# Kernel tuning notes

Hardware: AMD Instinct MI355X
Metric: run time of the kernel (lower is better)

The kernel has to match this reference:

```python
import jax, jax.numpy as jnp
import numpy as np

LEAKY_SLOPE = 0.2

def _xavier(key, shape, gain=1.414):
    a = gain * np.sqrt(6.0 / (shape[0] + shape[1]))
    return jax.random.uniform(key, shape, minval=-a, maxval=a, dtype=jnp.float32)

C_IN, HID = 64, 128
S_SCALES = [25, 12, 5]
T_SCALES = [64, 32, 16]

def setup_inputs() -> dict:
    key = jax.random.key(0)
    ks = jax.random.split(key, 32)
    B, T, J = 256, 64, 25
    d = {}
    d["src"] = jax.random.normal(ks[0], (B, C_IN, T, J), dtype=jnp.float32)
    d["W"] = _xavier(ks[1], (C_IN, HID))
    for i in range(3):
        d[f"as_src{i}"] = _xavier(ks[2 + i], (HID, 1))
        d[f"as_dst{i}"] = _xavier(ks[5 + i], (HID, 1))
        d[f"at_src{i}"] = _xavier(ks[8 + i], (HID, 1))
        d[f"at_dst{i}"] = _xavier(ks[11 + i], (HID, 1))
    # DiffPool assignment linears: in_features -> next_scale
    d["Wsp0"] = _xavier(ks[14], (C_IN, S_SCALES[1])); d["bsp0"] = jnp.zeros((S_SCALES[1],), jnp.float32)
    d["Wsp1"] = _xavier(ks[15], (C_IN, S_SCALES[2])); d["bsp1"] = jnp.zeros((S_SCALES[2],), jnp.float32)
    d["Wtp0"] = _xavier(ks[16], (C_IN, T_SCALES[1])); d["btp0"] = jnp.zeros((T_SCALES[1],), jnp.float32)
    d["Wtp1"] = _xavier(ks[17], (C_IN, T_SCALES[2])); d["btp1"] = jnp.zeros((T_SCALES[2],), jnp.float32)
    return d


def _gat_attn(emb, a_src, a_dst):
    # emb: [N, n, H]; additive GAT scores -> [N, n, n]
    s = emb @ a_src            # [N, n, 1]
    t = emb @ a_dst            # [N, n, 1]
    return jax.nn.leaky_relu(s + jnp.swapaxes(t, -1, -2), LEAKY_SLOPE)


def _diffpool(x, attn, Wp, bp):
    # assignment S = softmax(Linear(A @ X)) : [N, n, n_next]
    S = jax.nn.softmax((attn @ x) @ Wp + bp, axis=-1)
    x_next = jnp.einsum('bnk,bnc->bkc', S, x)
    return x_next, S


def _branch(x0, W, a_srcs, a_dsts, pool_params):
    n_scales = len(a_srcs)
    attns, pools = [], []
    x_cur = x0
    for i in range(n_scales):
        emb = x_cur @ W
        attns.append(_gat_attn(emb, a_srcs[i], a_dsts[i]))
        if i < n_scales - 1:
            Wp, bp = pool_params[i]
            x_cur, S = _diffpool(x_cur, attns[i], Wp, bp)
            pools.append(S)
    fusion = attns[0]
    for i in range(1, n_scales):
        S = pools[0]
        for j in range(1, i):
            S = S @ pools[j]
        fusion = fusion + S @ attns[i] @ jnp.swapaxes(S, -1, -2)
    # dropout is identity in eval mode
    return jax.nn.softmax(fusion, axis=-1)


def reference(src, W, as_src0, as_src1, as_src2, as_dst0, as_dst1, as_dst2,
              at_src0, at_src1, at_src2, at_dst0, at_dst1, at_dst2,
              Wsp0, bsp0, Wsp1, bsp1, Wtp0, btp0, Wtp1, btp1):
    B, C_in, T, J = src.shape
    x = jnp.transpose(src, (0, 2, 3, 1))              # [B, T, J, C]
    sp_x = x.reshape(B * T, J, C_in)                   # spatial graphs
    tp_x = jnp.transpose(x, (0, 2, 1, 3)).reshape(B * J, T, C_in)  # temporal graphs

    sa = _branch(sp_x, W, [as_src0, as_src1, as_src2], [as_dst0, as_dst1, as_dst2],
                 [(Wsp0, bsp0), (Wsp1, bsp1)])
    ta = _branch(tp_x, W, [at_src0, at_src1, at_src2], [at_dst0, at_dst1, at_dst2],
                 [(Wtp0, btp0), (Wtp1, btp1)])
    return sa.reshape(B, T, J, J), ta.reshape(B, J, T, T)
```

## Files before the change

### kernel.cpp

```cpp
#include <hip/hip_runtime.h>
#include <math.h>

constexpr float LEAKY = 0.2f;

__device__ __forceinline__ float4 ldf4(const float* p){ return *reinterpret_cast<const float4*>(p); }
__device__ __forceinline__ void stf4(float* p, float4 v){ *reinterpret_cast<float4*>(p) = v; }
__device__ __forceinline__ float dot4(float4 a, float4 b){ return a.x*b.x + a.y*b.y + a.z*b.z + a.w*b.w; }
__device__ __forceinline__ float4 fma4(float s, float4 b, float4 acc){
    acc.x += s*b.x; acc.y += s*b.y; acc.z += s*b.z; acc.w += s*b.w; return acc;
}
__device__ __forceinline__ float lrelu(float f){ return f > 0.f ? f : LEAKY*f; }
__device__ __forceinline__ float4 lrelu4(float s, float4 t){
    float4 r; r.x = lrelu(s+t.x); r.y = lrelu(s+t.y); r.z = lrelu(s+t.z); r.w = lrelu(s+t.w); return r;
}
__device__ __forceinline__ float vmax4(float4 v){ return fmaxf(fmaxf(v.x,v.y), fmaxf(v.z,v.w)); }
__device__ __forceinline__ float vsum4(float4 v){ return v.x+v.y+v.z+v.w; }
__device__ __forceinline__ float4 exp4(float4 a, float mx){
    float4 r; r.x = __expf(a.x-mx); r.y = __expf(a.y-mx); r.z = __expf(a.z-mx); r.w = __expf(a.w-mx); return r;
}

__global__ void prep_kernel(const float* __restrict__ W,
    const float* a0, const float* a1, const float* a2,  const float* a3,
    const float* a4, const float* a5, const float* a6,  const float* a7,
    const float* a8, const float* a9, const float* a10, const float* a11,
    const float* __restrict__ Wsp0, const float* __restrict__ Wsp1,
    const float* __restrict__ Wtp0, const float* __restrict__ Wtp1,
    float* __restrict__ ws)
{
    int blk = blockIdx.x, t = threadIdx.x;
    if (blk < 12) {
        const float* as[12] = {a0,a1,a2,a3,a4,a5,a6,a7,a8,a9,a10,a11};
        const float* a = as[blk];
        float s = 0.f;
        #pragma unroll
        for (int h = 0; h < 128; ++h) s += W[t*128 + h] * a[h];
        ws[blk*64 + t] = s;
    } else if (blk == 12) {
        for (int i = t; i < 768; i += 64) { int k = i >> 6, c = i & 63; ws[768 + i] = Wsp0[c*12 + k]; }
    } else if (blk == 13) {
        for (int i = t; i < 320; i += 64) { int k = i >> 6, c = i & 63; ws[1536 + i] = Wsp1[c*5 + k]; }
    } else if (blk == 14) {
        for (int i = t; i < 2048; i += 64) { int k = i >> 6, c = i & 63; ws[1856 + i] = Wtp0[c*32 + k]; }
    } else {
        for (int i = t; i < 1024; i += 64) { int k = i >> 6, c = i & 63; ws[3904 + i] = Wtp1[c*16 + k]; }
    }
}

__global__ __launch_bounds__(512, 4)
void temporal_kernel(const float* __restrict__ src, const float* __restrict__ wvec_g,
                     const float* __restrict__ Wp0, const float* __restrict__ b0,
                     const float* __restrict__ Wp1, const float* __restrict__ b1,
                     float* __restrict__ out, int nwg8)
{
    constexpr int NT = 512;
    constexpr int oA1 = 0;
    constexpr int oP1 = 1152;
    constexpr int oS1 = 1792;

    __shared__ __align__(16) float xr[4352];
    __shared__ __align__(16) float A0[4352];
    __shared__ __align__(16) float PR[2304];
    __shared__ __align__(16) float S0[2304];
    __shared__ __align__(16) float P01[1280];
    __shared__ __align__(16) float dv[256];
    __shared__ __align__(16) float sv[64], tv[64], rx[64], rs[64];
    __shared__ __align__(16) float ua[32], va[32];
    __shared__ __align__(16) float wv[384];

    const int tid = threadIdx.x;
    const int g = (blockIdx.x & 7) * nwg8 + (blockIdx.x >> 3);
    const int b = g / 25, inner = g - b*25;

    for (int i = tid; i < 384; i += NT) wv[i] = wvec_g[i];
    for (int i = tid; i < 4096; i += NT) {
        int c = i >> 6, r = i & 63;
        xr[r*68 + c] = src[((size_t)(b*64 + c)*64 + r)*25 + inner];
    }
    __syncthreads();

    for (int i = tid; i < 384; i += NT) {
        int which = i >> 6, p = i & 63;
        const float* w = wv + which*64;
        float acc = 0.f;
        #pragma unroll
        for (int c4 = 0; c4 < 16; ++c4) acc += dot4(ldf4(&xr[p*68 + 4*c4]), ldf4(&w[4*c4]));
        if (which == 0) sv[p] = acc;
        else if (which == 1) tv[p] = acc;
        else dv[(which-2)*64 + p] = acc;
    }
    for (int i = tid; i < 512; i += NT) {
        int p = i >> 3, k4 = i & 7;
        float4 acc = {0,0,0,0};
        #pragma unroll
        for (int c4 = 0; c4 < 16; ++c4) {
            float4 xv = ldf4(&xr[p*68 + 4*c4]);
            acc = fma4(xv.x, ldf4(&Wp0[(4*c4+0)*32 + 4*k4]), acc);
            acc = fma4(xv.y, ldf4(&Wp0[(4*c4+1)*32 + 4*k4]), acc);
            acc = fma4(xv.z, ldf4(&Wp0[(4*c4+2)*32 + 4*k4]), acc);
            acc = fma4(xv.w, ldf4(&Wp0[(4*c4+3)*32 + 4*k4]), acc);
        }
        stf4(&PR[p*36 + 4*k4], acc);
    }
    for (int i = tid; i < 256; i += NT) {
        int p = i >> 2, k4 = i & 3;
        float4 acc = {0,0,0,0};
        #pragma unroll
        for (int c4 = 0; c4 < 16; ++c4) {
            float4 xv = ldf4(&xr[p*68 + 4*c4]);
            acc = fma4(xv.x, ldf4(&Wp1[(4*c4+0)*16 + 4*k4]), acc);
            acc = fma4(xv.y, ldf4(&Wp1[(4*c4+1)*16 + 4*k4]), acc);
            acc = fma4(xv.z, ldf4(&Wp1[(4*c4+2)*16 + 4*k4]), acc);
            acc = fma4(xv.w, ldf4(&Wp1[(4*c4+3)*16 + 4*k4]), acc);
        }
        stf4(&P01[p*20 + 4*k4], acc);
    }
    __syncthreads();

    for (int i = tid; i < 1024; i += NT) {
        int p = i >> 4, q4 = i & 15;
        stf4(&A0[p*68 + 4*q4], lrelu4(sv[p], ldf4(&tv[4*q4])));
    }
    __syncthreads();

    if (tid < 128) {
        int p0 = tid >> 2, k8 = tid & 3;
        float4 a00 = ldf4(&b0[8*k8]), a01 = ldf4(&b0[8*k8 + 4]);
        float4 a10 = a00, a11 = a01;
        #pragma unroll
        for (int m4 = 0; m4 < 16; ++m4) {
            float4 av0 = ldf4(&A0[p0*68 + 4*m4]);
            float4 av1 = ldf4(&A0[(p0+32)*68 + 4*m4]);
            const float* f0 = (const float*)&av0;
            const float* f1 = (const float*)&av1;
            #pragma unroll
            for (int j = 0; j < 4; ++j) {
                float4 pr0 = ldf4(&PR[(4*m4+j)*36 + 8*k8]);
                float4 pr1 = ldf4(&PR[(4*m4+j)*36 + 8*k8 + 4]);
                a00 = fma4(f0[j], pr0, a00); a01 = fma4(f0[j], pr1, a01);
                a10 = fma4(f1[j], pr0, a10); a11 = fma4(f1[j], pr1, a11);
            }
        }
        stf4(&S0[p0*36 + 8*k8], a00);      stf4(&S0[p0*36 + 8*k8 + 4], a01);
        stf4(&S0[(p0+32)*36 + 8*k8], a10); stf4(&S0[(p0+32)*36 + 8*k8 + 4], a11);
    }
    __syncthreads();

    {
        int p = tid >> 3, l = tid & 7;
        float4 v = ldf4(&S0[p*36 + 4*l]);
        float mx = vmax4(v);
        mx = fmaxf(mx, __shfl_xor(mx,1)); mx = fmaxf(mx, __shfl_xor(mx,2)); mx = fmaxf(mx, __shfl_xor(mx,4));
        v = exp4(v, mx);
        float sm = vsum4(v);
        sm += __shfl_xor(sm,1); sm += __shfl_xor(sm,2); sm += __shfl_xor(sm,4);
        float inv = 1.f/sm;
        v.x *= inv; v.y *= inv; v.z *= inv; v.w *= inv;
        stf4(&S0[p*36 + 4*l], v);
    }
    __syncthreads();

    if (tid < 128) {
        int k = tid >> 2, j4 = tid & 3;
        float4 acc = {0,0,0,0};
        #pragma unroll
        for (int p = 0; p < 64; ++p)
            acc = fma4(S0[p*36 + k], ldf4(&P01[p*20 + 4*j4]), acc);
        stf4(&xr[oP1 + k*20 + 4*j4], acc);
    } else if (tid < 256) {
        int i = tid - 128;
        int j = i >> 5, k = i & 31;
        const float* d = dv + j*64;
        float acc = 0.f;
        #pragma unroll
        for (int p = 0; p < 64; ++p) acc += S0[p*36 + k] * d[p];
        if (j == 0) sv[k] = acc; else if (j == 1) tv[k] = acc;
        else if (j == 2) ua[k] = acc; else va[k] = acc;
    }
    __syncthreads();

    for (int i = tid; i < 1024; i += NT) {
        int p = i >> 5, q = i & 31;
        xr[oA1 + p*36 + q] = lrelu(sv[p] + tv[q]);
    }
    __syncthreads();

    for (int i = tid; i < 128; i += NT) {
        int p = i >> 2, k4 = i & 3;
        float4 acc = ldf4(&b1[4*k4]);
        #pragma unroll
        for (int m = 0; m < 32; ++m) acc = fma4(xr[oA1 + p*36 + m], ldf4(&xr[oP1 + m*20 + 4*k4]), acc);
        stf4(&xr[oS1 + p*20 + 4*k4], acc);
    }
    __syncthreads();

    if (tid < 128) {
        int m = tid >> 2, l = tid & 3;
        float4 v = ldf4(&xr[oS1 + m*20 + 4*l]);
        float mx = vmax4(v);
        mx = fmaxf(mx, __shfl_xor(mx,1)); mx = fmaxf(mx, __shfl_xor(mx,2));
        v = exp4(v, mx);
        float sm = vsum4(v);
        sm += __shfl_xor(sm,1); sm += __shfl_xor(sm,2);
        float inv = 1.f/sm;
        v.x *= inv; v.y *= inv; v.z *= inv; v.w *= inv;
        stf4(&xr[oS1 + m*20 + 4*l], v);
    }
    __syncthreads();

    for (int k = tid; k < 16; k += NT) {
        float a = 0.f, c2 = 0.f;
        #pragma unroll
        for (int n = 0; n < 32; ++n) { float s1 = xr[oS1 + n*20 + k]; a += s1*ua[n]; c2 += s1*va[n]; }
        rx[k] = a; rs[k] = c2;
    }
    __syncthreads();

    {
        int m = tid >> 4, k = tid & 15;
        float rsk = rs[k];
        float acc = 0.f;
        #pragma unroll
        for (int j = 0; j < 16; ++j)
            acc += xr[oS1 + m*20 + j] * lrelu(rx[j] + rsk);
        xr[oP1 + m*20 + k] = acc;
    }
    __syncthreads();

    for (int i = tid; i < 1024; i += NT) {
        int m = i >> 5, n = i & 31;
        float acc = xr[oA1 + m*36 + n];
        #pragma unroll
        for (int j4 = 0; j4 < 4; ++j4)
            acc += dot4(ldf4(&xr[oP1 + m*20 + 4*j4]), ldf4(&xr[oS1 + n*20 + 4*j4]));
        xr[oA1 + m*36 + n] = acc;
    }
    __syncthreads();

    for (int i = tid; i < 512; i += NT) {
        int p = i >> 3, k4 = i & 7;
        float4 acc = {0,0,0,0};
        #pragma unroll
        for (int m = 0; m < 32; ++m) acc = fma4(S0[p*36 + m], ldf4(&xr[oA1 + m*36 + 4*k4]), acc);
        stf4(&PR[p*36 + 4*k4], acc);
    }
    __syncthreads();

    {
        int q = tid & 63, pg = tid >> 6;
        float4 s0r[8];
        #pragma unroll
        for (int j = 0; j < 8; ++j) s0r[j] = ldf4(&S0[q*36 + 4*j]);
        #pragma unroll
        for (int pi = 0; pi < 8; ++pi) {
            int p = pg*8 + pi;
            float acc = 0.f;
            #pragma unroll
            for (int j = 0; j < 8; ++j) acc += dot4(ldf4(&PR[p*36 + 4*j]), s0r[j]);
            A0[p*68 + q] += acc;
        }
    }
    __syncthreads();

    {
        int p = tid >> 3, l = tid & 7;
        float4 v1 = ldf4(&A0[p*68 + 4*l]);
        float4 v2 = ldf4(&A0[p*68 + 32 + 4*l]);
        float mx = fmaxf(vmax4(v1), vmax4(v2));
        mx = fmaxf(mx, __shfl_xor(mx,1)); mx = fmaxf(mx, __shfl_xor(mx,2)); mx = fmaxf(mx, __shfl_xor(mx,4));
        float4 e1 = exp4(v1, mx), e2 = exp4(v2, mx);
        float sm = vsum4(e1) + vsum4(e2);
        sm += __shfl_xor(sm,1); sm += __shfl_xor(sm,2); sm += __shfl_xor(sm,4);
        float inv = 1.f/sm;
        e1.x*=inv; e1.y*=inv; e1.z*=inv; e1.w*=inv;
        e2.x*=inv; e2.y*=inv; e2.z*=inv; e2.w*=inv;
        size_t base = (size_t)g*4096 + (size_t)p*64;
        stf4(&out[base + 4*l], e1);
        stf4(&out[base + 32 + 4*l], e2);
    }
}

__global__ __launch_bounds__(256, 4)
void spatial_kernel(const float* __restrict__ src, const float* __restrict__ wvg,
                    const float* __restrict__ WpT0, const float* __restrict__ WpT1,
                    const float* __restrict__ b0, const float* __restrict__ b1,
                    float* __restrict__ out, int nwg8)
{
    __shared__ __align__(16) float Rx0[1700];
    __shared__ __align__(16) float RA0[700];
    __shared__ __align__(16) float RPR[816];
    __shared__ __align__(16) float RS0[500];
    __shared__ __align__(16) float sv[32], tv[32], ua[32], va[32], rxa[8], rsa[8];

    float* x0  = Rx0;
    float* A1  = Rx0;
    float* A1T = Rx0 + 240;
    float* P1T = Rx0 + 480;
    float* S1  = Rx0 + 540;
    float* T1  = Rx0 + 744;
    float* A0  = RA0;
    float* P0T = RPR;
    float* x1  = RPR;
    float* M1  = RPR;
    float* S0  = RS0;

    const int t = threadIdx.x;
    const int g = (blockIdx.x & 7) * nwg8 + (blockIdx.x >> 3);
    const int b = g >> 6, inner = g & 63;
    const float* srcb = src + (size_t)b*102400 + inner*25;

    for (int i = t; i < 400; i += 256) {
        int r = i % 25, c0 = (i / 25) << 2;
        float4 v;
        v.x = srcb[(c0+0)*1600 + r];
        v.y = srcb[(c0+1)*1600 + r];
        v.z = srcb[(c0+2)*1600 + r];
        v.w = srcb[(c0+3)*1600 + r];
        stf4(&x0[r*68 + c0], v);
    }
    __syncthreads();

    if (t < 50) {
        int which = t / 25, p = t - which*25;
        const float* w = wvg + which*64;
        float a = 0.f;
        #pragma unroll
        for (int c4 = 0; c4 < 16; ++c4) a += dot4(ldf4(&x0[p*68 + 4*c4]), ldf4(&w[4*c4]));
        if (which) tv[p] = a; else sv[p] = a;
    }
    for (int i = t; i < 336; i += 256) {
        int k = i / 28, m = i - k*28;
        float a = 0.f;
        if (m < 25) {
            #pragma unroll
            for (int c4 = 0; c4 < 16; ++c4) a += dot4(ldf4(&WpT0[k*64 + 4*c4]), ldf4(&x0[m*68 + 4*c4]));
        }
        P0T[k*28 + m] = a;
    }
    __syncthreads();

    for (int i = t; i < 700; i += 256) {
        int p = i / 28, q = i - p*28;
        A0[i] = (q < 25) ? lrelu(sv[p] + tv[q]) : -1e30f;
    }
    __syncthreads();

    for (int i = t; i < 300; i += 256) {
        int p = i / 12, k = i - p*12;
        float acc = b0[k];
        #pragma unroll
        for (int m4 = 0; m4 < 7; ++m4) acc += dot4(ldf4(&A0[p*28 + 4*m4]), ldf4(&P0T[k*28 + 4*m4]));
        S0[p*20 + k] = acc;
    }
    __syncthreads();

    if (t < 25) {
        float4 r[3]; float mx = -1e30f;
        #pragma unroll
        for (int u = 0; u < 3; ++u) { r[u] = ldf4(&S0[t*20 + 4*u]); mx = fmaxf(mx, vmax4(r[u])); }
        float sm = 0.f;
        #pragma unroll
        for (int u = 0; u < 3; ++u) { r[u] = exp4(r[u], mx); sm += vsum4(r[u]); }
        float inv = 1.f/sm;
        #pragma unroll
        for (int u = 0; u < 3; ++u) {
            r[u].x *= inv; r[u].y *= inv; r[u].z *= inv; r[u].w *= inv;
            stf4(&S0[t*20 + 4*u], r[u]);
        }
    }
    __syncthreads();

    if (t < 96) {
        int k = t >> 3, c0 = (t & 7) << 3;
        float4 a = {0,0,0,0}, bb = {0,0,0,0};
        #pragma unroll
        for (int p = 0; p < 25; ++p) {
            float s = S0[p*20 + k];
            a  = fma4(s, ldf4(&x0[p*68 + c0]), a);
            bb = fma4(s, ldf4(&x0[p*68 + c0 + 4]), bb);
        }
        stf4(&x1[k*68 + c0], a);
        stf4(&x1[k*68 + c0 + 4], bb);
    }
    __syncthreads();

    if (t < 48) {
        int which = t / 12, p = t - which*12;
        const float* w = wvg + (2+which)*64;
        float a = 0.f;
        #pragma unroll
        for (int c4 = 0; c4 < 16; ++c4) a += dot4(ldf4(&x1[p*68 + 4*c4]), ldf4(&w[4*c4]));
        if (which == 0) sv[p] = a; else if (which == 1) tv[p] = a;
        else if (which == 2) ua[p] = a; else va[p] = a;
    }
    for (int i = t; i < 60; i += 256) {
        int j = i / 12, k = i - j*12;
        float a = 0.f;
        #pragma unroll
        for (int c4 = 0; c4 < 16; ++c4) a += dot4(ldf4(&WpT1[j*64 + 4*c4]), ldf4(&x1[k*68 + 4*c4]));
        P1T[j*12 + k] = a;
    }
    __syncthreads();

    for (int i = t; i < 288; i += 256) {
        int mat = i / 144, rr = (i - mat*144) / 12, q = i % 12;
        if (mat == 0) A1 [rr*20 + q] = lrelu(sv[rr] + tv[q]);
        else          A1T[rr*20 + q] = lrelu(sv[q] + tv[rr]);
    }
    __syncthreads();

    for (int i = t; i < 60; i += 256) {
        int m = i / 5, j = i - m*5;
        float acc = b1[j];
        #pragma unroll
        for (int k4 = 0; k4 < 3; ++k4) acc += dot4(ldf4(&A1[m*20 + 4*k4]), ldf4(&P1T[j*12 + 4*k4]));
        S1[m*12 + j] = acc;
    }
    __syncthreads();

    if (t < 12) {
        float mx = -1e30f;
        float r0 = S1[t*12+0], r1 = S1[t*12+1], r2 = S1[t*12+2], r3 = S1[t*12+3], r4 = S1[t*12+4];
        mx = fmaxf(fmaxf(fmaxf(r0,r1), fmaxf(r2,r3)), r4);
        r0 = __expf(r0-mx); r1 = __expf(r1-mx); r2 = __expf(r2-mx); r3 = __expf(r3-mx); r4 = __expf(r4-mx);
        float inv = 1.f/(r0+r1+r2+r3+r4);
        S1[t*12+0] = r0*inv; S1[t*12+1] = r1*inv; S1[t*12+2] = r2*inv; S1[t*12+3] = r3*inv; S1[t*12+4] = r4*inv;
    }
    __syncthreads();

    if (t < 10) {
        int which = t / 5, k = t - which*5;
        float a = 0.f;
        #pragma unroll
        for (int n = 0; n < 12; ++n) a += S1[n*12 + k] * (which ? va[n] : ua[n]);
        if (which) rsa[k] = a; else rxa[k] = a;
    }
    __syncthreads();

    if (t < 60) {
        int m = t / 5, k = t - m*5;
        float rsk = rsa[k];
        float acc = 0.f;
        #pragma unroll
        for (int j = 0; j < 5; ++j) acc += S1[m*12 + j] * lrelu(rxa[j] + rsk);
        T1[m*5 + k] = acc;
    }
    __syncthreads();

    if (t < 144) {
        int m = t / 12, n = t - m*12;
        float acc = A1[m*20 + n];
        #pragma unroll
        for (int j = 0; j < 5; ++j) acc += T1[m*5 + j] * S1[n*12 + j];
        A1[m*20 + n] = acc;
        A1T[n*20 + m] = acc;
    }
    __syncthreads();

    for (int i = t; i < 300; i += 256) {
        int p = i / 12, k = i - p*12;
        float acc = 0.f;
        #pragma unroll
        for (int m4 = 0; m4 < 3; ++m4) acc += dot4(ldf4(&S0[p*20 + 4*m4]), ldf4(&A1T[k*20 + 4*m4]));
        M1[p*20 + k] = acc;
    }
    __syncthreads();

    for (int i = t; i < 625; i += 256) {
        int p = i / 25, q = i - p*25;
        float acc = A0[p*28 + q];
        #pragma unroll
        for (int m4 = 0; m4 < 3; ++m4) acc += dot4(ldf4(&M1[p*20 + 4*m4]), ldf4(&S0[q*20 + 4*m4]));
        A0[p*28 + q] = acc;
    }
    __syncthreads();

    if (t < 25) {
        float4 r[7]; float mx = -1e30f;
        #pragma unroll
        for (int u = 0; u < 7; ++u) { r[u] = ldf4(&A0[t*28 + 4*u]); mx = fmaxf(mx, vmax4(r[u])); }
        float sm = 0.f;
        #pragma unroll
        for (int u = 0; u < 7; ++u) sm += vsum4(exp4(r[u], mx));
        sv[t] = mx; tv[t] = 1.f/sm;
    }
    __syncthreads();

    for (int i = t; i < 625; i += 256) {
        int p = i / 25, q = i - p*25;
        out[(size_t)g*625 + i] = __expf(A0[p*28 + q] - sv[p]) * tv[p];
    }
}

extern "C" void kernel_launch(void* const* d_in, const int* in_sizes, int n_in,
                              void* d_out, int out_size, void* d_ws, size_t ws_size,
                              hipStream_t stream) {
    const float* src = (const float*)d_in[0];
    const float* W   = (const float*)d_in[1];
    float* ws = (float*)d_ws;

    prep_kernel<<<16, 64, 0, stream>>>(W,
        (const float*)d_in[2],  (const float*)d_in[3],
        (const float*)d_in[6],  (const float*)d_in[7],
        (const float*)d_in[10], (const float*)d_in[11],
        (const float*)d_in[4],  (const float*)d_in[5],
        (const float*)d_in[8],  (const float*)d_in[9],
        (const float*)d_in[12], (const float*)d_in[13],
        (const float*)d_in[14], (const float*)d_in[16],
        (const float*)d_in[18], (const float*)d_in[20],
        ws);

    float* out = (float*)d_out;
    spatial_kernel<<<16384, 256, 0, stream>>>(
        src, ws, ws + 768, ws + 1536,
        (const float*)d_in[15], (const float*)d_in[17],
        out, 16384/8);
    temporal_kernel<<<6400, 512, 0, stream>>>(
        src, ws + 384,
        (const float*)d_in[18], (const float*)d_in[19],
        (const float*)d_in[20], (const float*)d_in[21],
        out + 10240000, 6400/8);
}
```

Baseline: 438.9 us.

## Store transposed S0 in shared memory and register-tile temporal small matmuls

The temporal kernel now writes a transposed copy of the softmaxed assignment matrix S0 into extra shared memory. Several small matmuls (S0^T·P01, S0^T·d, S0·A1, PR·S0^T) are rewritten as 2x2 float4 register-blocked tiles that read vectorized rows from this copy, replacing strided scalar reads. The projection dot products are also merged so one thread computes all six per row. This aims to cut LDS instruction count and bank conflicts, at the cost of more shared memory per block (which may affect occupancy) and fewer active threads in those phases.

New measurement: 440.3 us. About the same (+0.3%).

```diff
diff --git a/kernel.cpp b/kernel.cpp
--- a/kernel.cpp
+++ b/kernel.cpp
@@ -56,8 +56,9 @@
     constexpr int oA1 = 0;
     constexpr int oP1 = 1152;
     constexpr int oS1 = 1792;
-
-    __shared__ __align__(16) float xr[4352];
+    constexpr int oS0T = 2432;
+
+    __shared__ __align__(16) float xr[4608];
     __shared__ __align__(16) float A0[4352];
     __shared__ __align__(16) float PR[2304];
     __shared__ __align__(16) float S0[2304];
@@ -78,15 +79,16 @@
     }
     __syncthreads();
 
-    for (int i = tid; i < 384; i += NT) {
-        int which = i >> 6, p = i & 63;
-        const float* w = wv + which*64;
-        float acc = 0.f;
-        #pragma unroll
-        for (int c4 = 0; c4 < 16; ++c4) acc += dot4(ldf4(&xr[p*68 + 4*c4]), ldf4(&w[4*c4]));
-        if (which == 0) sv[p] = acc;
-        else if (which == 1) tv[p] = acc;
-        else dv[(which-2)*64 + p] = acc;
+    if (tid < 64) {
+        float acc[6] = {};
+        #pragma unroll
+        for (int c4 = 0; c4 < 16; ++c4) {
+            float4 xv = ldf4(&xr[tid*68 + 4*c4]);
+            #pragma unroll
+            for (int d = 0; d < 6; ++d) acc[d] += dot4(xv, ldf4(&wv[d*64 + 4*c4]));
+        }
+        sv[tid] = acc[0]; tv[tid] = acc[1];
+        dv[tid] = acc[2]; dv[64+tid] = acc[3]; dv[128+tid] = acc[4]; dv[192+tid] = acc[5];
     }
     for (int i = tid; i < 512; i += NT) {
         int p = i >> 3, k4 = i & 7;
@@ -156,23 +158,39 @@
         float inv = 1.f/sm;
         v.x *= inv; v.y *= inv; v.z *= inv; v.w *= inv;
         stf4(&S0[p*36 + 4*l], v);
-    }
-    __syncthreads();
-
-    if (tid < 128) {
-        int k = tid >> 2, j4 = tid & 3;
-        float4 acc = {0,0,0,0};
-        #pragma unroll
-        for (int p = 0; p < 64; ++p)
-            acc = fma4(S0[p*36 + k], ldf4(&P01[p*20 + 4*j4]), acc);
-        stf4(&xr[oP1 + k*20 + 4*j4], acc);
-    } else if (tid < 256) {
-        int i = tid - 128;
+        xr[oS0T + (4*l+0)*68 + p] = v.x;
+        xr[oS0T + (4*l+1)*68 + p] = v.y;
+        xr[oS0T + (4*l+2)*68 + p] = v.z;
+        xr[oS0T + (4*l+3)*68 + p] = v.w;
+    }
+    __syncthreads();
+
+    if (tid < 64) {
+        int k0 = tid >> 2, j4 = tid & 3;
+        float4 acc0 = {0,0,0,0}, acc1 = {0,0,0,0};
+        #pragma unroll
+        for (int p4 = 0; p4 < 16; ++p4) {
+            float4 s0 = ldf4(&xr[oS0T + k0*68 + 4*p4]);
+            float4 s1 = ldf4(&xr[oS0T + (k0+16)*68 + 4*p4]);
+            const float* f0 = (const float*)&s0;
+            const float* f1 = (const float*)&s1;
+            #pragma unroll
+            for (int j = 0; j < 4; ++j) {
+                float4 pv = ldf4(&P01[(4*p4+j)*20 + 4*j4]);
+                acc0 = fma4(f0[j], pv, acc0);
+                acc1 = fma4(f1[j], pv, acc1);
+            }
+        }
+        stf4(&xr[oP1 + k0*20 + 4*j4], acc0);
+        stf4(&xr[oP1 + (k0+16)*20 + 4*j4], acc1);
+    } else if (tid < 192) {
+        int i = tid - 64;
         int j = i >> 5, k = i & 31;
         const float* d = dv + j*64;
         float acc = 0.f;
         #pragma unroll
-        for (int p = 0; p < 64; ++p) acc += S0[p*36 + k] * d[p];
+        for (int p4 = 0; p4 < 16; ++p4)
+            acc += dot4(ldf4(&xr[oS0T + k*68 + 4*p4]), ldf4(&d[4*p4]));
         if (j == 0) sv[k] = acc; else if (j == 1) tv[k] = acc;
         else if (j == 2) ua[k] = acc; else va[k] = acc;
     }
@@ -236,28 +254,50 @@
     }
     __syncthreads();
 
-    for (int i = tid; i < 512; i += NT) {
-        int p = i >> 3, k4 = i & 7;
-        float4 acc = {0,0,0,0};
-        #pragma unroll
-        for (int m = 0; m < 32; ++m) acc = fma4(S0[p*36 + m], ldf4(&xr[oA1 + m*36 + 4*k4]), acc);
-        stf4(&PR[p*36 + 4*k4], acc);
-    }
-    __syncthreads();
-
-    {
-        int q = tid & 63, pg = tid >> 6;
-        float4 s0r[8];
-        #pragma unroll
-        for (int j = 0; j < 8; ++j) s0r[j] = ldf4(&S0[q*36 + 4*j]);
-        #pragma unroll
-        for (int pi = 0; pi < 8; ++pi) {
-            int p = pg*8 + pi;
-            float acc = 0.f;
+    if (tid < 128) {
+        int p0 = tid >> 2, k8 = tid & 3;
+        float4 a00 = {0,0,0,0}, a01 = {0,0,0,0}, a10 = {0,0,0,0}, a11 = {0,0,0,0};
+        #pragma unroll
+        for (int m4 = 0; m4 < 8; ++m4) {
+            float4 av0 = ldf4(&S0[p0*36 + 4*m4]);
+            float4 av1 = ldf4(&S0[(p0+32)*36 + 4*m4]);
+            const float* f0 = (const float*)&av0;
+            const float* f1 = (const float*)&av1;
             #pragma unroll
-            for (int j = 0; j < 8; ++j) acc += dot4(ldf4(&PR[p*36 + 4*j]), s0r[j]);
-            A0[p*68 + q] += acc;
-        }
+            for (int j = 0; j < 4; ++j) {
+                float4 b0v = ldf4(&xr[oA1 + (4*m4+j)*36 + 8*k8]);
+                float4 b1v = ldf4(&xr[oA1 + (4*m4+j)*36 + 8*k8 + 4]);
+                a00 = fma4(f0[j], b0v, a00); a01 = fma4(f0[j], b1v, a01);
+                a10 = fma4(f1[j], b0v, a10); a11 = fma4(f1[j], b1v, a11);
+            }
+        }
+        stf4(&PR[p0*36 + 8*k8], a00);      stf4(&PR[p0*36 + 8*k8 + 4], a01);
+        stf4(&PR[(p0+32)*36 + 8*k8], a10); stf4(&PR[(p0+32)*36 + 8*k8 + 4], a11);
+    }
+    __syncthreads();
+
+    if (tid < 256) {
+        int p0 = tid >> 3, q8 = tid & 7;
+        float4 a00 = ldf4(&A0[p0*68 + 8*q8]);
+        float4 a01 = ldf4(&A0[p0*68 + 8*q8 + 4]);
+        float4 a10 = ldf4(&A0[(p0+32)*68 + 8*q8]);
+        float4 a11 = ldf4(&A0[(p0+32)*68 + 8*q8 + 4]);
+        #pragma unroll
+        for (int m4 = 0; m4 < 8; ++m4) {
+            float4 av0 = ldf4(&PR[p0*36 + 4*m4]);
+            float4 av1 = ldf4(&PR[(p0+32)*36 + 4*m4]);
+            const float* f0 = (const float*)&av0;
+            const float* f1 = (const float*)&av1;
+            #pragma unroll
+            for (int j = 0; j < 4; ++j) {
+                float4 s0v = ldf4(&xr[oS0T + (4*m4+j)*68 + 8*q8]);
+                float4 s1v = ldf4(&xr[oS0T + (4*m4+j)*68 + 8*q8 + 4]);
+                a00 = fma4(f0[j], s0v, a00); a01 = fma4(f0[j], s1v, a01);
+                a10 = fma4(f1[j], s0v, a10); a11 = fma4(f1[j], s1v, a11);
+            }
+        }
+        stf4(&A0[p0*68 + 8*q8], a00);      stf4(&A0[p0*68 + 8*q8 + 4], a01);
+        stf4(&A0[(p0+32)*68 + 8*q8], a10); stf4(&A0[(p0+32)*68 + 8*q8 + 4], a11);
     }
     __syncthreads();
 
```
